# Kernel optimization log

Hardware: AMD Instinct MI355X
Metric: run time of the kernel (lower is better)

The kernel has to match this reference:

```python
import jax, jax.numpy as jnp
import numpy as np

Q_NODES = 100000
S_NODES = 100000
N_EDGES = 3200000
D = 3
HIDDEN = 64
OUT_DIM = 128
STAT_DIM = 3 + 2 * D  # N_i, D_avg, D_var, Delta(D), PCA(D)


def setup_inputs() -> dict:
    key = jax.random.key(0)
    ks = jax.random.split(key, 7)
    source_pos = jax.random.normal(ks[0], (S_NODES, D), dtype=jnp.float32)
    query_pos = jax.random.normal(ks[1], (Q_NODES, D), dtype=jnp.float32)
    qi = jax.random.randint(ks[2], (N_EDGES,), 0, Q_NODES, dtype=jnp.int64)
    si = jax.random.randint(ks[3], (N_EDGES,), 0, S_NODES, dtype=jnp.int64)
    edge_index = jnp.stack([qi, si], axis=0)
    # MLP params (torch Linear default-ish scale)
    W1 = jax.random.normal(ks[4], (HIDDEN, STAT_DIM), dtype=jnp.float32) / np.sqrt(STAT_DIM)
    b1 = jnp.zeros((HIDDEN,), dtype=jnp.float32)
    W2 = jax.random.normal(ks[5], (OUT_DIM, HIDDEN), dtype=jnp.float32) / np.sqrt(HIDDEN)
    b2 = jnp.zeros((OUT_DIM,), dtype=jnp.float32)
    return {"source_pos": source_pos, "query_pos": query_pos, "edge_index": edge_index,
            "W1": W1, "b1": b1, "W2": W2, "b2": b2}


def _stat_features(source_pos, query_pos, edge_index):
    Q = query_pos.shape[0]
    qi = edge_index[0]
    si = edge_index[1]
    ones = jnp.ones(qi.shape, dtype=jnp.float32)
    counts = jax.ops.segment_sum(ones, qi, num_segments=Q)          # [Q] = N_i
    has = counts > 0
    Nc = jnp.where(has, counts, 1.0)                                 # clamp 0 -> 1

    nbr = source_pos[si]                                             # [E,D]
    qc = query_pos[qi]                                               # [E,D]
    dist = jnp.linalg.norm(nbr - qc, axis=1)                         # [E]
    D_avg = jax.ops.segment_sum(dist, qi, num_segments=Q) / Nc       # [Q]
    E_X2 = jax.ops.segment_sum(dist * dist, qi, num_segments=Q) / Nc
    D_var = jnp.maximum(E_X2 - D_avg * D_avg, 0.0)

    centroid = jax.ops.segment_sum(nbr, qi, num_segments=Q) / Nc[:, None]  # [Q,D]
    Delta = centroid - query_pos                                     # [Q,D]

    centered = nbr - centroid[qi]                                    # [E,D]
    cov_comp = centered[:, :, None] * centered[:, None, :]           # [E,D,D]
    cov = jax.ops.segment_sum(cov_comp, qi, num_segments=Q) / Nc[:, None, None]

    eig = jnp.linalg.eigvalsh(cov)[:, ::-1]                          # descending [Q,D]
    PCA = jnp.where(has[:, None], eig, 0.0)

    feats = jnp.concatenate([counts[:, None], D_avg[:, None], D_var[:, None], Delta, PCA], axis=1)
    feats = jnp.where(has[:, None], feats, 0.0)

    mean = feats.mean(axis=0, keepdims=True)
    std = jnp.std(feats, axis=0, ddof=1, keepdims=True)              # torch std is unbiased
    std = jnp.where(std < 1e-6, 1.0, std)
    return (feats - mean) / std


def reference(source_pos, query_pos, edge_index, W1, b1, W2, b2):
    feats = _stat_features(source_pos, query_pos, edge_index)        # [Q, 9]
    h = jax.nn.relu(feats @ W1.T + b1)
    return h @ W2.T + b2                                             # [Q, OUT_DIM]
```

## Files before the change

### kernel.cpp

```cpp
#include <hip/hip_runtime.h>
#include <math.h>

#define Q_NODES 100000
#define S_NODES 100000
#define N_EDGES 3200000
#define HIDDEN 64
#define OUT_DIM 128

#define QPB   128
#define NB    782
#define CAPB  4608
#define TILE  4096
#define NT4   (N_EDGES / 4)

#define F_CURSOR_OFF 0
#define F_NORM_OFF   3200
#define F_PSUM_OFF   3328
#define F_PSUMSQ_OFF 31488
#define F_FEATS_OFF  59648
#define F_SP4_OFF    3659648
#define F_SLOTS_OFF  5259648
#define F_ZERO_BYTES 3200
#define F_WS_NEED    (5259648ull + (unsigned long long)(NB * CAPB + 1) * 4)

#define B_ACC_OFF    0
#define B_STATS_OFF  4800000
#define B_NORM_OFF   4800144
#define B_FEATS_OFF  4800224
#define B_ZERO_BYTES 4800144

__device__ __forceinline__ void atomAddF(float* p, float v) {
#if defined(__gfx950__) || defined(__gfx942__) || defined(__gfx90a__)
    unsafeAtomicAdd(p, v);
#else
    atomicAdd(p, v);
#endif
}


__device__ __forceinline__ void eig3_sym(
        float a00, float a01, float a02, float a11, float a12, float a22,
        float& e1, float& e2, float& e3) {
    float p1 = a01 * a01 + a02 * a02 + a12 * a12;
    float qm = (a00 + a11 + a22) * (1.0f / 3.0f);
    float b00 = a00 - qm, b11 = a11 - qm, b22 = a22 - qm;
    float p2 = b00 * b00 + b11 * b11 + b22 * b22 + 2.0f * p1;
    if (p2 <= 1e-24f) {
        e1 = qm; e2 = qm; e3 = qm;
    } else {
        float p = sqrtf(p2 * (1.0f / 6.0f));
        float invp = 1.0f / p;
        float c00 = b00 * invp, c11 = b11 * invp, c22 = b22 * invp;
        float c01 = a01 * invp, c02 = a02 * invp, c12 = a12 * invp;
        float detB = c00 * (c11 * c22 - c12 * c12)
                   - c01 * (c01 * c22 - c12 * c02)
                   + c02 * (c01 * c12 - c11 * c02);
        float r = 0.5f * detB;
        r = fminf(fmaxf(r, -1.0f), 1.0f);
        float phi = acosf(r) * (1.0f / 3.0f);
        e1 = qm + 2.0f * p * cosf(phi);
        e3 = qm + 2.0f * p * cosf(phi + 2.0943951023931953f);
        e2 = 3.0f * qm - e1 - e3;
    }
}

__device__ __forceinline__ void sums_to_feats(
        const float* s, float qx, float qy, float qz, float* f) {
    float n = s[0];
#pragma unroll
    for (int k = 0; k < 9; ++k) f[k] = 0.0f;
    if (n > 0.0f) {
        float inv = 1.0f / n;
        float Davg = s[1] * inv;
        float Dvar = fmaxf(s[2] * inv - Davg * Davg, 0.0f);
        float cx = s[3] * inv, cy = s[4] * inv, cz = s[5] * inv;
        float a00 = fmaxf(s[6] * inv - cx * cx, 0.0f);
        float a01 = s[7] * inv - cx * cy;
        float a02 = s[8] * inv - cx * cz;
        float a11 = fmaxf(s[9] * inv - cy * cy, 0.0f);
        float a12 = s[10] * inv - cy * cz;
        float a22 = fmaxf(s[11] * inv - cz * cz, 0.0f);
        float e1, e2, e3;
        eig3_sym(a00, a01, a02, a11, a12, a22, e1, e2, e3);
        f[0] = n; f[1] = Davg; f[2] = Dvar;
        f[3] = cx - qx; f[4] = cy - qy; f[5] = cz - qz;
        f[6] = e1; f[7] = e2; f[8] = e3;
    }
}


__global__ __launch_bounds__(256) void pad_kernel(
        const float* __restrict__ sp, float4* __restrict__ sp4) {
    int i = blockIdx.x * 256 + threadIdx.x;
    if (i < S_NODES) sp4[i] = make_float4(sp[3 * i], sp[3 * i + 1], sp[3 * i + 2], 0.0f);
}

__global__ __launch_bounds__(256) void partition_kernel(
        const int* __restrict__ edge,
        int* __restrict__ cursor,
        unsigned int* __restrict__ slots) {
    __shared__ unsigned int s_rec[TILE];
    __shared__ int s_pos[TILE];
    __shared__ int s_hist[NB];
    __shared__ int s_cur[NB];
    __shared__ int s_off[NB];
    __shared__ int s_wsum[4];

    int tid = threadIdx.x;
    int lane = tid & 63, wv = tid >> 6;
    int tileStart = blockIdx.x * TILE;
    int tileCount = N_EDGES - tileStart;
    if (tileCount > TILE) tileCount = TILE;

    for (int b = tid; b < NB; b += 256) s_hist[b] = 0;
    __syncthreads();

    const int4* eq4 = (const int4*)edge;
    const int4* es4 = (const int4*)(edge + N_EDGES);
    int base4 = blockIdx.x * (TILE / 4);
    int4 q4[4], s4[4];
    bool v[4];
#pragma unroll
    for (int j = 0; j < 4; ++j) {
        int i4 = base4 + tid + j * 256;
        v[j] = i4 < NT4;
        int ic = v[j] ? i4 : 0;
        q4[j] = eq4[ic];
        s4[j] = es4[ic];
        if (v[j]) {
            atomicAdd(&s_hist[q4[j].x >> 7], 1);
            atomicAdd(&s_hist[q4[j].y >> 7], 1);
            atomicAdd(&s_hist[q4[j].z >> 7], 1);
            atomicAdd(&s_hist[q4[j].w >> 7], 1);
        }
    }
    __syncthreads();

    int local[4], tsum = 0;
#pragma unroll
    for (int j = 0; j < 4; ++j) {
        int idx = 4 * tid + j;
        local[j] = (idx < NB) ? s_hist[idx] : 0;
        tsum += local[j];
    }
    int inc = tsum;
#pragma unroll
    for (int off = 1; off < 64; off <<= 1) {
        int t = __shfl_up(inc, off);
        if (lane >= off) inc += t;
    }
    if (lane == 63) s_wsum[wv] = inc;
    __syncthreads();
    int wbase = 0;
    for (int w = 0; w < wv; ++w) wbase += s_wsum[w];
    int run = wbase + inc - tsum;
#pragma unroll
    for (int j = 0; j < 4; ++j) {
        int idx = 4 * tid + j;
        if (idx < NB) s_cur[idx] = run;
        run += local[j];
    }
    __syncthreads();

    for (int b = tid; b < NB; b += 256) {
        int c = s_hist[b];
        int base = c ? atomicAdd(&cursor[b], c) : 0;
        s_off[b] = b * CAPB + base - s_cur[b];
    }
    __syncthreads();

#pragma unroll
    for (int j = 0; j < 4; ++j) {
        if (v[j]) {
            int qs[4] = { q4[j].x, q4[j].y, q4[j].z, q4[j].w };
            int ss[4] = { s4[j].x, s4[j].y, s4[j].z, s4[j].w };
#pragma unroll
            for (int m = 0; m < 4; ++m) {
                int bkt = qs[m] >> 7;
                int idx = atomicAdd(&s_cur[bkt], 1);
                int gpos = idx + s_off[bkt];
                if (gpos >= (bkt + 1) * CAPB) gpos = NB * CAPB;
                s_rec[idx] = ((unsigned)(qs[m] & (QPB - 1)) << 17) | (unsigned)ss[m];
                s_pos[idx] = gpos;
            }
        }
    }
    __syncthreads();

    for (int i = tid; i < tileCount; i += 256)
        slots[s_pos[i]] = s_rec[i];
}

__global__ __launch_bounds__(256) void bucket_kernel(
        const int* __restrict__ cursor,
        const unsigned int* __restrict__ slots,
        const float4* __restrict__ sp4,
        const float* __restrict__ qp,
        float* __restrict__ feats,
        float* __restrict__ psum,
        float* __restrict__ psumsq) {
    __shared__ unsigned int s_sorted[CAPB];
    __shared__ float qtile[QPB * 3];
    __shared__ int s_cnt[QPB], s_start[QPB], s_cur[QPB];
    __shared__ float s_red1[4][9], s_red2[4][9];

    int tid = threadIdx.x;
    int b = blockIdx.x;
    int cnt = cursor[b];
    if (cnt > CAPB) cnt = CAPB;

    if (tid < QPB) s_cnt[tid] = 0;
    for (int i = tid; i < QPB * 3; i += 256) {
        int g = b * QPB * 3 + i;
        qtile[i] = (g < Q_NODES * 3) ? qp[g] : 0.0f;
    }
    __syncthreads();

    const unsigned int* bslots = slots + b * CAPB;
    for (int i = tid; i < cnt; i += 256)
        atomicAdd(&s_cnt[bslots[i] >> 17], 1);
    __syncthreads();

    if (tid < 64) {
        int a0 = s_cnt[tid], a1 = s_cnt[64 + tid];
        int i0 = a0, i1 = a1;
#pragma unroll
        for (int off = 1; off < 64; off <<= 1) {
            int t0 = __shfl_up(i0, off); if (tid >= off) i0 += t0;
            int t1 = __shfl_up(i1, off); if (tid >= off) i1 += t1;
        }
        int tot0 = __shfl(i0, 63);
        s_start[tid] = i0 - a0;              s_cur[tid] = i0 - a0;
        s_start[64 + tid] = i1 - a1 + tot0;  s_cur[64 + tid] = i1 - a1 + tot0;
    }
    __syncthreads();

    for (int i = tid; i < cnt; i += 256) {
        unsigned rec = bslots[i];
        int pos = atomicAdd(&s_cur[rec >> 17], 1);
        s_sorted[pos] = rec;
    }
    __syncthreads();

    float f[9];
#pragma unroll
    for (int k = 0; k < 9; ++k) f[k] = 0.0f;
    int q = b * QPB + tid;
    if (tid < QPB && q < Q_NODES) {
        float qx = qtile[3 * tid + 0], qy = qtile[3 * tid + 1], qz = qtile[3 * tid + 2];
        float s[12];
#pragma unroll
        for (int k = 0; k < 12; ++k) s[k] = 0.0f;
        int st = s_start[tid], deg = s_cnt[tid];
        for (int j = 0; j < deg; ++j) {
            unsigned rec = s_sorted[st + j];
            float4 sv = sp4[rec & 0x1FFFF];
            float dx = sv.x - qx, dy = sv.y - qy, dz = sv.z - qz;
            float d2 = dx * dx + dy * dy + dz * dz;
            s[0] += 1.0f;
            s[1] += sqrtf(d2);
            s[2] += d2;
            s[3] += sv.x; s[4] += sv.y; s[5] += sv.z;
            s[6] += sv.x * sv.x; s[7] += sv.x * sv.y; s[8] += sv.x * sv.z;
            s[9] += sv.y * sv.y; s[10] += sv.y * sv.z; s[11] += sv.z * sv.z;
        }
        sums_to_feats(s, qx, qy, qz, f);
#pragma unroll
        for (int k = 0; k < 9; ++k) feats[k * Q_NODES + q] = f[k];
    }

    int lane = tid & 63, wv = tid >> 6;
#pragma unroll
    for (int k = 0; k < 9; ++k) {
        float s1 = f[k];
        float s2 = f[k] * f[k];
#pragma unroll
        for (int off = 32; off > 0; off >>= 1) {
            s1 += __shfl_down(s1, off);
            s2 += __shfl_down(s2, off);
        }
        if (lane == 0) { s_red1[wv][k] = s1; s_red2[wv][k] = s2; }
    }
    __syncthreads();
    if (tid < 9) {
        psum[tid * NB + b]   = s_red1[0][tid] + s_red1[1][tid] + s_red1[2][tid] + s_red1[3][tid];
        psumsq[tid * NB + b] = s_red2[0][tid] + s_red2[1][tid] + s_red2[2][tid] + s_red2[3][tid];
    }
}

__global__ __launch_bounds__(256) void stats_reduce_kernel(
        const float* __restrict__ psum,
        const float* __restrict__ psumsq,
        float* __restrict__ norm) {
    __shared__ double w1[4], w2[4];
    int tid = threadIdx.x, lane = tid & 63, wv = tid >> 6;
    for (int k = 0; k < 9; ++k) {
        double a1 = 0.0, a2 = 0.0;
        for (int b = tid; b < NB; b += 256) {
            a1 += (double)psum[k * NB + b];
            a2 += (double)psumsq[k * NB + b];
        }
#pragma unroll
        for (int off = 32; off > 0; off >>= 1) {
            a1 += __shfl_down(a1, off);
            a2 += __shfl_down(a2, off);
        }
        if (lane == 0) { w1[wv] = a1; w2[wv] = a2; }
        __syncthreads();
        if (tid == 0) {
            double S  = w1[0] + w1[1] + w1[2] + w1[3];
            double S2 = w2[0] + w2[1] + w2[2] + w2[3];
            double mean = S / (double)Q_NODES;
            double var = (S2 - S * S / (double)Q_NODES) / (double)(Q_NODES - 1);
            if (var < 0.0) var = 0.0;
            double sd = sqrt(var);
            if (sd < 1e-6) sd = 1.0;
            norm[k] = (float)mean;
            norm[9 + k] = (float)(1.0 / sd);
        }
        __syncthreads();
    }
}


__global__ __launch_bounds__(256, 3) void mlp_kernel(
        const float* __restrict__ feats,
        const float* __restrict__ norm,
        const float* __restrict__ W1, const float* __restrict__ b1,
        const float* __restrict__ W2, const float* __restrict__ b2,
        float* __restrict__ out) {
    __shared__ float sW1[576];
    __shared__ float sB1[64];
    __shared__ float sB2[64];
    __shared__ float sNorm[18];
    __shared__ float w2t[64 * 64];
    __shared__ float ht[64 * 128];

    int tid = threadIdx.x;
    int blk_q = blockIdx.x >> 1;
    int oh = (blockIdx.x & 1) * 64;

    for (int i = tid; i < 576; i += 256) sW1[i] = W1[i];
    if (tid < 64) { sB1[tid] = b1[tid]; sB2[tid] = b2[oh + tid]; }
    if (tid < 18) sNorm[tid] = norm[tid];
    __syncthreads();

    {
        int o = tid & 63, kc = (tid >> 6) * 16;
#pragma unroll
        for (int j = 0; j < 16; ++j) {
            int k = kc + j;
            w2t[k * 64 + o] = W2[(oh + o) * 64 + k];
        }
    }

    {
        int q = tid & 127, half = tid >> 7;
        int qg = blk_q * 128 + q;
        int qc = qg < Q_NODES ? qg : Q_NODES - 1;
        float f[9];
#pragma unroll
        for (int k = 0; k < 9; ++k)
            f[k] = (feats[k * Q_NODES + qc] - sNorm[k]) * sNorm[9 + k];
#pragma unroll 4
        for (int j = 0; j < 32; ++j) {
            int ko = half * 32 + j;
            float a = sB1[ko];
#pragma unroll
            for (int kf = 0; kf < 9; ++kf) a = fmaf(f[kf], sW1[ko * 9 + kf], a);
            ht[ko * 128 + q] = fmaxf(a, 0.0f);
        }
    }
    __syncthreads();

    int qt = tid >> 4, ot = tid & 15;
    int q0 = qt * 8, o0 = ot * 4;
    float acc[8][4];
#pragma unroll
    for (int i = 0; i < 8; ++i)
#pragma unroll
        for (int j = 0; j < 4; ++j) acc[i][j] = 0.0f;

#pragma unroll 4
    for (int k = 0; k < 64; ++k) {
        float4 h0 = *(const float4*)&ht[k * 128 + q0];
        float4 h1 = *(const float4*)&ht[k * 128 + q0 + 4];
        float4 w  = *(const float4*)&w2t[k * 64 + o0];
        float hh[8] = { h0.x, h0.y, h0.z, h0.w, h1.x, h1.y, h1.z, h1.w };
#pragma unroll
        for (int i = 0; i < 8; ++i) {
            acc[i][0] = fmaf(hh[i], w.x, acc[i][0]);
            acc[i][1] = fmaf(hh[i], w.y, acc[i][1]);
            acc[i][2] = fmaf(hh[i], w.z, acc[i][2]);
            acc[i][3] = fmaf(hh[i], w.w, acc[i][3]);
        }
    }

    float4 bb = *(const float4*)&sB2[o0];
#pragma unroll
    for (int i = 0; i < 8; ++i) {
        int qg = blk_q * 128 + q0 + i;
        if (qg < Q_NODES) {
            float4 v = make_float4(acc[i][0] + bb.x, acc[i][1] + bb.y,
                                   acc[i][2] + bb.z, acc[i][3] + bb.w);
            *(float4*)(out + (size_t)qg * 128 + oh + o0) = v;
        }
    }
}


__global__ __launch_bounds__(256) void edge_kernel(
        const int* __restrict__ edge,
        const float* __restrict__ sp,
        const float* __restrict__ qp,
        float* __restrict__ acc) {
    int e = blockIdx.x * 256 + threadIdx.x;
    if (e >= N_EDGES) return;
    int q = edge[e];
    int s = edge[N_EDGES + e];
    float sx = sp[3 * s + 0], sy = sp[3 * s + 1], sz = sp[3 * s + 2];
    float qx = qp[3 * q + 0], qy = qp[3 * q + 1], qz = qp[3 * q + 2];
    float dx = sx - qx, dy = sy - qy, dz = sz - qz;
    float d2 = dx * dx + dy * dy + dz * dz;
    atomAddF(acc + 0 * Q_NODES + q, 1.0f);
    atomAddF(acc + 1 * Q_NODES + q, sqrtf(d2));
    atomAddF(acc + 2 * Q_NODES + q, d2);
    atomAddF(acc + 3 * Q_NODES + q, sx);
    atomAddF(acc + 4 * Q_NODES + q, sy);
    atomAddF(acc + 5 * Q_NODES + q, sz);
    atomAddF(acc + 6 * Q_NODES + q, sx * sx);
    atomAddF(acc + 7 * Q_NODES + q, sx * sy);
    atomAddF(acc + 8 * Q_NODES + q, sx * sz);
    atomAddF(acc + 9 * Q_NODES + q, sy * sy);
    atomAddF(acc + 10 * Q_NODES + q, sy * sz);
    atomAddF(acc + 11 * Q_NODES + q, sz * sz);
}

__global__ __launch_bounds__(256) void finalize_kernel(
        const float* __restrict__ acc,
        const float* __restrict__ qp,
        float* __restrict__ feats,
        double* __restrict__ stats) {
    int q = blockIdx.x * 256 + threadIdx.x;
    float f[9];
#pragma unroll
    for (int k = 0; k < 9; ++k) f[k] = 0.0f;
    if (q < Q_NODES) {
        float s[12];
#pragma unroll
        for (int k = 0; k < 12; ++k) s[k] = acc[k * Q_NODES + q];
        float qx = qp[3 * q + 0], qy = qp[3 * q + 1], qz = qp[3 * q + 2];
        sums_to_feats(s, qx, qy, qz, f);
#pragma unroll
        for (int k = 0; k < 9; ++k) feats[k * Q_NODES + q] = f[k];
    }
    int lane = threadIdx.x & 63;
#pragma unroll
    for (int k = 0; k < 9; ++k) {
        float s1 = f[k];
        float s2 = f[k] * f[k];
#pragma unroll
        for (int off = 32; off > 0; off >>= 1) {
            s1 += __shfl_down(s1, off);
            s2 += __shfl_down(s2, off);
        }
        if (lane == 0) {
            atomicAdd(&stats[k], (double)s1);
            atomicAdd(&stats[9 + k], (double)s2);
        }
    }
}

__global__ void stats_kernel(const double* __restrict__ stats,
                             float* __restrict__ norm) {
    int k = threadIdx.x;
    if (k < 9) {
        double S = stats[k], S2 = stats[9 + k];
        double mean = S / (double)Q_NODES;
        double var = (S2 - S * S / (double)Q_NODES) / (double)(Q_NODES - 1);
        if (var < 0.0) var = 0.0;
        double sd = sqrt(var);
        if (sd < 1e-6) sd = 1.0;
        norm[k] = (float)mean;
        norm[9 + k] = (float)(1.0 / sd);
    }
}


extern "C" void kernel_launch(void* const* d_in, const int* in_sizes, int n_in,
                              void* d_out, int out_size, void* d_ws, size_t ws_size,
                              hipStream_t stream) {
    const float* sp   = (const float*)d_in[0];
    const float* qp   = (const float*)d_in[1];
    const int*   edge = (const int*)d_in[2];
    const float* W1   = (const float*)d_in[3];
    const float* b1   = (const float*)d_in[4];
    const float* W2   = (const float*)d_in[5];
    const float* b2   = (const float*)d_in[6];
    float* out = (float*)d_out;
    char* ws = (char*)d_ws;

    if (ws_size >= F_WS_NEED) {
        int*          cursor = (int*)(ws + F_CURSOR_OFF);
        float*        norm   = (float*)(ws + F_NORM_OFF);
        float*        psum   = (float*)(ws + F_PSUM_OFF);
        float*        psumsq = (float*)(ws + F_PSUMSQ_OFF);
        float*        feats  = (float*)(ws + F_FEATS_OFF);
        float4*       sp4    = (float4*)(ws + F_SP4_OFF);
        unsigned int* slots  = (unsigned int*)(ws + F_SLOTS_OFF);

        hipMemsetAsync(ws, 0, F_ZERO_BYTES, stream);
        pad_kernel<<<(S_NODES + 255) / 256, 256, 0, stream>>>(sp, sp4);
        partition_kernel<<<(N_EDGES + TILE - 1) / TILE, 256, 0, stream>>>(edge, cursor, slots);
        bucket_kernel<<<NB, 256, 0, stream>>>(cursor, slots, sp4, qp, feats, psum, psumsq);
        stats_reduce_kernel<<<1, 256, 0, stream>>>(psum, psumsq, norm);
        mlp_kernel<<<NB * 2, 256, 0, stream>>>(feats, norm, W1, b1, W2, b2, out);
    } else {
        float*  acc   = (float*)(ws + B_ACC_OFF);
        double* stats = (double*)(ws + B_STATS_OFF);
        float*  norm  = (float*)(ws + B_NORM_OFF);
        float*  feats = (float*)(ws + B_FEATS_OFF);

        hipMemsetAsync(ws, 0, B_ZERO_BYTES, stream);
        edge_kernel<<<N_EDGES / 256, 256, 0, stream>>>(edge, sp, qp, acc);
        finalize_kernel<<<(Q_NODES + 255) / 256, 256, 0, stream>>>(acc, qp, feats, stats);
        stats_kernel<<<1, 64, 0, stream>>>(stats, norm);
        mlp_kernel<<<NB * 2, 256, 0, stream>>>(feats, norm, W1, b1, W2, b2, out);
    }
}
```

Before: 206.6 us.

## Split bucket gather across all threads and compute full MLP output per block

In bucket_kernel, both halves of the 256-thread block now walk each query's neighbor list (even/odd edges), and the partial sums are combined through shared memory. Before, only 128 threads did the gather work. The MLP kernel now computes all 128 output columns per block with an 8x8 register tile, which halves the grid and avoids recomputing the hidden layer twice per query tile. The cost is more shared memory and registers in the MLP (launch bounds lowered to 2 blocks), plus an extra shared-memory reduction step in the bucket kernel.

```diff
diff --git a/kernel.cpp b/kernel.cpp
--- a/kernel.cpp
+++ b/kernel.cpp
@@ -201,6 +201,7 @@
         float* __restrict__ psumsq) {
     __shared__ unsigned int s_sorted[CAPB];
     __shared__ float qtile[QPB * 3];
+    __shared__ float s_part[QPB * 13];
     __shared__ int s_cnt[QPB], s_start[QPB], s_cur[QPB];
     __shared__ float s_red1[4][9], s_red2[4][9];
 
@@ -242,17 +243,15 @@
     }
     __syncthreads();
 
-    float f[9];
-#pragma unroll
-    for (int k = 0; k < 9; ++k) f[k] = 0.0f;
-    int q = b * QPB + tid;
-    if (tid < QPB && q < Q_NODES) {
-        float qx = qtile[3 * tid + 0], qy = qtile[3 * tid + 1], qz = qtile[3 * tid + 2];
-        float s[12];
-#pragma unroll
-        for (int k = 0; k < 12; ++k) s[k] = 0.0f;
-        int st = s_start[tid], deg = s_cnt[tid];
-        for (int j = 0; j < deg; ++j) {
+    int qloc = tid & 127, half = tid >> 7;
+    float s[12];
+#pragma unroll
+    for (int k = 0; k < 12; ++k) s[k] = 0.0f;
+    {
+        float qx = qtile[3 * qloc + 0], qy = qtile[3 * qloc + 1], qz = qtile[3 * qloc + 2];
+        int st = s_start[qloc], deg = s_cnt[qloc];
+#pragma unroll 4
+        for (int j = half; j < deg; j += 2) {
             unsigned rec = s_sorted[st + j];
             float4 sv = sp4[rec & 0x1FFFF];
             float dx = sv.x - qx, dy = sv.y - qy, dz = sv.z - qz;
@@ -264,7 +263,21 @@
             s[6] += sv.x * sv.x; s[7] += sv.x * sv.y; s[8] += sv.x * sv.z;
             s[9] += sv.y * sv.y; s[10] += sv.y * sv.z; s[11] += sv.z * sv.z;
         }
-        sums_to_feats(s, qx, qy, qz, f);
+    }
+    if (half == 1) {
+#pragma unroll
+        for (int k = 0; k < 12; ++k) s_part[qloc * 13 + k] = s[k];
+    }
+    __syncthreads();
+
+    float f[9];
+#pragma unroll
+    for (int k = 0; k < 9; ++k) f[k] = 0.0f;
+    int q = b * QPB + qloc;
+    if (half == 0 && q < Q_NODES) {
+#pragma unroll
+        for (int k = 0; k < 12; ++k) s[k] += s_part[qloc * 13 + k];
+        sums_to_feats(s, qtile[3 * qloc + 0], qtile[3 * qloc + 1], qtile[3 * qloc + 2], f);
 #pragma unroll
         for (int k = 0; k < 9; ++k) feats[k * Q_NODES + q] = f[k];
     }
@@ -323,7 +336,7 @@
 }
 
 
-__global__ __launch_bounds__(256, 3) void mlp_kernel(
+__global__ __launch_bounds__(256, 2) void mlp_kernel(
         const float* __restrict__ feats,
         const float* __restrict__ norm,
         const float* __restrict__ W1, const float* __restrict__ b1,
@@ -331,28 +344,31 @@
         float* __restrict__ out) {
     __shared__ float sW1[576];
     __shared__ float sB1[64];
-    __shared__ float sB2[64];
+    __shared__ float sB2[128];
     __shared__ float sNorm[18];
-    __shared__ float w2t[64 * 64];
+    __shared__ float w2t[64 * 128];
     __shared__ float ht[64 * 128];
 
     int tid = threadIdx.x;
-    int blk_q = blockIdx.x >> 1;
-    int oh = (blockIdx.x & 1) * 64;
+    int blk_q = blockIdx.x;
 
     for (int i = tid; i < 576; i += 256) sW1[i] = W1[i];
-    if (tid < 64) { sB1[tid] = b1[tid]; sB2[tid] = b2[oh + tid]; }
+    if (tid < 64) sB1[tid] = b1[tid];
+    if (tid < 128) sB2[tid] = b2[tid];
     if (tid < 18) sNorm[tid] = norm[tid];
-    __syncthreads();
 
     {
-        int o = tid & 63, kc = (tid >> 6) * 16;
-#pragma unroll
-        for (int j = 0; j < 16; ++j) {
-            int k = kc + j;
-            w2t[k * 64 + o] = W2[(oh + o) * 64 + k];
-        }
-    }
+        int o = tid & 127, kc = (tid >> 7) * 32;
+#pragma unroll
+        for (int j = 0; j < 32; j += 4) {
+            float4 w = *(const float4*)&W2[o * 64 + kc + j];
+            w2t[(kc + j + 0) * 128 + o] = w.x;
+            w2t[(kc + j + 1) * 128 + o] = w.y;
+            w2t[(kc + j + 2) * 128 + o] = w.z;
+            w2t[(kc + j + 3) * 128 + o] = w.w;
+        }
+    }
+    __syncthreads();
 
     {
         int q = tid & 127, half = tid >> 7;
@@ -374,36 +390,39 @@
     __syncthreads();
 
     int qt = tid >> 4, ot = tid & 15;
-    int q0 = qt * 8, o0 = ot * 4;
-    float acc[8][4];
+    int q0 = qt * 8, o0 = ot * 8;
+    float acc[8][8];
 #pragma unroll
     for (int i = 0; i < 8; ++i)
 #pragma unroll
-        for (int j = 0; j < 4; ++j) acc[i][j] = 0.0f;
-
-#pragma unroll 4
+        for (int j = 0; j < 8; ++j) acc[i][j] = 0.0f;
+
+#pragma unroll 2
     for (int k = 0; k < 64; ++k) {
         float4 h0 = *(const float4*)&ht[k * 128 + q0];
         float4 h1 = *(const float4*)&ht[k * 128 + q0 + 4];
-        float4 w  = *(const float4*)&w2t[k * 64 + o0];
+        float4 w0 = *(const float4*)&w2t[k * 128 + o0];
+        float4 w1 = *(const float4*)&w2t[k * 128 + o0 + 4];
         float hh[8] = { h0.x, h0.y, h0.z, h0.w, h1.x, h1.y, h1.z, h1.w };
-#pragma unroll
-        for (int i = 0; i < 8; ++i) {
-            acc[i][0] = fmaf(hh[i], w.x, acc[i][0]);
-            acc[i][1] = fmaf(hh[i], w.y, acc[i][1]);
-            acc[i][2] = fmaf(hh[i], w.z, acc[i][2]);
-            acc[i][3] = fmaf(hh[i], w.w, acc[i][3]);
-        }
-    }
-
-    float4 bb = *(const float4*)&sB2[o0];
+        float ww[8] = { w0.x, w0.y, w0.z, w0.w, w1.x, w1.y, w1.z, w1.w };
+#pragma unroll
+        for (int i = 0; i < 8; ++i)
+#pragma unroll
+            for (int j = 0; j < 8; ++j)
+                acc[i][j] = fmaf(hh[i], ww[j], acc[i][j]);
+    }
+
+    float4 bb0 = *(const float4*)&sB2[o0];
+    float4 bb1 = *(const float4*)&sB2[o0 + 4];
 #pragma unroll
     for (int i = 0; i < 8; ++i) {
         int qg = blk_q * 128 + q0 + i;
         if (qg < Q_NODES) {
-            float4 v = make_float4(acc[i][0] + bb.x, acc[i][1] + bb.y,
-                                   acc[i][2] + bb.z, acc[i][3] + bb.w);
-            *(float4*)(out + (size_t)qg * 128 + oh + o0) = v;
+            float* op = out + (size_t)qg * 128 + o0;
+            *(float4*)op = make_float4(acc[i][0] + bb0.x, acc[i][1] + bb0.y,
+                                       acc[i][2] + bb0.z, acc[i][3] + bb0.w);
+            *(float4*)(op + 4) = make_float4(acc[i][4] + bb1.x, acc[i][5] + bb1.y,
+                                             acc[i][6] + bb1.z, acc[i][7] + bb1.w);
         }
     }
 }
@@ -514,7 +533,7 @@
         partition_kernel<<<(N_EDGES + TILE - 1) / TILE, 256, 0, stream>>>(edge, cursor, slots);
         bucket_kernel<<<NB, 256, 0, stream>>>(cursor, slots, sp4, qp, feats, psum, psumsq);
         stats_reduce_kernel<<<1, 256, 0, stream>>>(psum, psumsq, norm);
-        mlp_kernel<<<NB * 2, 256, 0, stream>>>(feats, norm, W1, b1, W2, b2, out);
+        mlp_kernel<<<NB, 256, 0, stream>>>(feats, norm, W1, b1, W2, b2, out);
     } else {
         float*  acc   = (float*)(ws + B_ACC_OFF);
         double* stats = (double*)(ws + B_STATS_OFF);
@@ -525,6 +544,6 @@
         edge_kernel<<<N_EDGES / 256, 256, 0, stream>>>(edge, sp, qp, acc);
         finalize_kernel<<<(Q_NODES + 255) / 256, 256, 0, stream>>>(acc, qp, feats, stats);
         stats_kernel<<<1, 64, 0, stream>>>(stats, norm);
-        mlp_kernel<<<NB * 2, 256, 0, stream>>>(feats, norm, W1, b1, W2, b2, out);
-    }
-}
+        mlp_kernel<<<NB, 256, 0, stream>>>(feats, norm, W1, b1, W2, b2, out);
+    }
+}
```

Result: no change. 208.1 us (+0.8%).
